# Optimization experiments

Measured on AMD Instinct MI355X. Metric: run time of the kernel, lower is better.

## Reference

```python
import jax, jax.numpy as jnp
import numpy as np
import math

WS = 8      # window size
HEADS = 8

def _layer_norm(x, g, b, eps=1e-5):
    m = jnp.mean(x, -1, keepdims=True)
    v = jnp.var(x, -1, keepdims=True)
    return (x - m) / jnp.sqrt(v + eps) * g + b

def _freqs_cis_2d(dim, end, theta=10000.0):
    # 2D axial RoPE: half the rotary dims encode row, half encode column of a sqrt(end) grid
    H = int(math.sqrt(end))
    nf = dim // 4
    freqs = 1.0 / (theta ** (np.arange(0, dim, 4)[:nf].astype(np.float32) / dim))
    f = np.outer(np.arange(H, dtype=np.float32), freqs)          # [H, dim/4]
    fh = np.broadcast_to(f[:, None, :], (H, H, nf))
    fw = np.broadcast_to(f[None, :, :], (H, H, nf))
    ang = np.concatenate([fh, fw], -1).reshape(end, dim // 2)    # [end, dim/2]
    return jnp.asarray(np.cos(ang)), jnp.asarray(np.sin(ang))

def _apply_rope(t, cos, sin):
    # t: [B, n, h, d], cos/sin: [n, d/2]; adjacent pairs form complex numbers (torch view_as_complex)
    tr, ti = t[..., 0::2], t[..., 1::2]
    c = cos[None, :, None, :]
    s = sin[None, :, None, :]
    outr = tr * c - ti * s
    outi = tr * s + ti * c
    return jnp.stack([outr, outi], -1).reshape(t.shape)

def _rel_pos_index(ws):
    coords = np.stack(np.meshgrid(np.arange(ws), np.arange(ws), indexing='ij')).reshape(2, -1)
    rel = (coords[:, :, None] - coords[:, None, :]).transpose(1, 2, 0)
    rel[..., 0] += ws - 1
    rel[..., 1] += ws - 1
    rel[..., 0] *= 2 * ws - 1
    return rel.sum(-1)  # [ws^2, ws^2]

def _rel_coords_table(ws):
    r = np.arange(-(ws - 1), ws, dtype=np.float32)
    t = np.stack(np.meshgrid(r, r, indexing='ij'), -1)  # [2ws-1, 2ws-1, 2]
    t = t / (ws - 1)
    t = t * 8.0
    t = np.sign(t) * np.log2(np.abs(t) + 1.0) / np.log2(8.0)
    return t.reshape(-1, 2)

def _cosine_attn(q, k, v, ls, bias=None):
    # v2 attention: cosine-normalized QK with clamped learnable logit scale
    qn = q / jnp.clip(jnp.linalg.norm(q, axis=-1, keepdims=True), 1e-12)
    kn = k / jnp.clip(jnp.linalg.norm(k, axis=-1, keepdims=True), 1e-12)
    a = jnp.einsum('bhnd,bhmd->bhnm', qn, kn) * jnp.exp(jnp.minimum(ls, 4.6052))
    if bias is not None:
        a = a + bias
    a = jax.nn.softmax(a, -1)
    return jnp.einsum('bhnm,bhmd->bhnd', a, v)

def _window_partition(x, ws):
    B, H, W, C = x.shape
    x = x.reshape(B, H // ws, ws, W // ws, ws, C).transpose(0, 1, 3, 2, 4, 5)
    return x.reshape(-1, ws * ws, C)

def _window_reverse(xw, ws, H, W, C):
    x = xw.reshape(-1, H // ws, W // ws, ws, ws, C).transpose(0, 1, 3, 2, 4, 5)
    return x.reshape(-1, H, W, C)

def setup_inputs() -> dict:
    key = jax.random.key(0)
    ks = jax.random.split(key, 12)
    B, H, W, C, heads, mr = 8, 64, 64, 512, HEADS, 4
    nct = (H // WS) * (W // WS)  # one carrier token per window, 8x8 grid
    s = 0.02
    d = {}
    d['x'] = jax.random.normal(ks[0], (B, H, W, C), jnp.float32)
    d['ct'] = jax.random.normal(ks[1], (B, nct, C), jnp.float32)
    d['w_qkv_ct'] = jax.random.normal(ks[2], (C, 3 * C), jnp.float32) * s
    d['logit_scale_ct'] = jnp.full((heads, 1, 1), float(np.log(10.0)), jnp.float32)
    d['ln_g_ct1'] = jnp.ones(C); d['ln_b_ct1'] = jnp.zeros(C)
    d['ln_g_ct2'] = jnp.ones(C); d['ln_b_ct2'] = jnp.zeros(C)
    d['mlp_ct_w1'] = jax.random.normal(ks[3], (C, mr * C), jnp.float32) * s
    d['mlp_ct_b1'] = jnp.zeros(mr * C)
    d['mlp_ct_w2'] = jax.random.normal(ks[4], (mr * C, C), jnp.float32) * s
    d['mlp_ct_b2'] = jnp.zeros(C)
    d['w_qkv_win'] = jax.random.normal(ks[5], (C, 3 * C), jnp.float32) * s
    d['w_proj_win'] = jax.random.normal(ks[6], (C, C), jnp.float32) * s
    d['b_proj_win'] = jnp.zeros(C)
    d['logit_scale_win'] = jnp.full((heads, 1, 1), float(np.log(10.0)), jnp.float32)
    d['ln_g_w1'] = jnp.ones(C); d['ln_b_w1'] = jnp.zeros(C)
    d['ln_g_w2'] = jnp.ones(C); d['ln_b_w2'] = jnp.zeros(C)
    d['cpb_w1'] = jax.random.normal(ks[7], (2, 512), jnp.float32) * s
    d['cpb_b1'] = jnp.zeros(512)
    d['cpb_w2'] = jax.random.normal(ks[8], (512, heads), jnp.float32) * s
    d['mlp_w_w1'] = jax.random.normal(ks[9], (C, mr * C), jnp.float32) * s
    d['mlp_w_b1'] = jnp.zeros(mr * C)
    d['mlp_w_w2'] = jax.random.normal(ks[10], (mr * C, C), jnp.float32) * s
    d['mlp_w_b2'] = jnp.zeros(C)
    return d

def reference(x, ct, w_qkv_ct, logit_scale_ct, ln_g_ct1, ln_b_ct1, ln_g_ct2, ln_b_ct2,
              mlp_ct_w1, mlp_ct_b1, mlp_ct_w2, mlp_ct_b2,
              w_qkv_win, w_proj_win, b_proj_win, logit_scale_win,
              ln_g_w1, ln_b_w1, ln_g_w2, ln_b_w2,
              cpb_w1, cpb_b1, cpb_w2,
              mlp_w_w1, mlp_w_b1, mlp_w_w2, mlp_w_b2):
    B, H, W, C = x.shape
    heads = HEADS
    hd = C // heads
    n_ct = ct.shape[1]

    # ---- carrier-token global attention (RoPE2d + cosine-scaled QK, v2) ----
    h = _layer_norm(ct, ln_g_ct1, ln_b_ct1)
    q, k, v = jnp.split(h @ w_qkv_ct, 3, -1)
    q = q.reshape(B, n_ct, heads, hd)
    k = k.reshape(B, n_ct, heads, hd)
    cos, sin = _freqs_cis_2d(hd, n_ct)
    q = _apply_rope(q, cos, sin).transpose(0, 2, 1, 3)   # [B,h,n,d]
    k = _apply_rope(k, cos, sin).transpose(0, 2, 1, 3)
    v = v.reshape(B, n_ct, heads, hd).transpose(0, 2, 1, 3)
    o = _cosine_attn(q, k, v, logit_scale_ct)
    ct = ct + o.transpose(0, 2, 1, 3).reshape(B, n_ct, C)
    h = _layer_norm(ct, ln_g_ct2, ln_b_ct2)
    ct = ct + (jax.nn.gelu(h @ mlp_ct_w1 + mlp_ct_b1, approximate=False) @ mlp_ct_w2 + mlp_ct_b2)

    # ---- windowed local attention with carrier token prepended per window ----
    xw = _window_partition(x, WS)          # [B*nW, ws^2, C]
    ctw = ct.reshape(-1, 1, C)             # carrier token for each window
    z = jnp.concatenate([ctw, xw], 1)      # [B*nW, 1+ws^2, C]
    N = z.shape[1]
    h2 = _layer_norm(z, ln_g_w1, ln_b_w1)
    q, k, v = jnp.split(h2 @ w_qkv_win, 3, -1)
    q = q.reshape(-1, N, heads, hd).transpose(0, 2, 1, 3)
    k = k.reshape(-1, N, heads, hd).transpose(0, 2, 1, 3)
    v = v.reshape(-1, N, heads, hd).transpose(0, 2, 1, 3)

    # Swin-v2 log-CPB relative position bias, zero-padded for the global (carrier) token
    table = jnp.asarray(_rel_coords_table(WS))
    tb = jax.nn.relu(table @ cpb_w1 + cpb_b1) @ cpb_w2          # [(2ws-1)^2, heads]
    rpi = _rel_pos_index(WS).reshape(-1)
    bias = tb[rpi].reshape(WS * WS, WS * WS, heads).transpose(2, 0, 1)
    bias = 16.0 * jax.nn.sigmoid(bias)
    ng = N - WS * WS
    bias = jnp.pad(bias, ((0, 0), (ng, 0), (ng, 0)))

    o = _cosine_attn(q, k, v, logit_scale_win, bias[None])
    o = o.transpose(0, 2, 1, 3).reshape(-1, N, C)
    z = z + (o @ w_proj_win + b_proj_win)
    h2 = _layer_norm(z, ln_g_w2, ln_b_w2)
    z = z + (jax.nn.gelu(h2 @ mlp_w_w1 + mlp_w_b1, approximate=False) @ mlp_w_w2 + mlp_w_b2)

    x_out = _window_reverse(z[:, 1:, :], WS, H, W, C)   # [B,H,W,C]
    return x_out
```

## Files before the change

### kernel.cpp

```cpp
#include <hip/hip_runtime.h>
#include <math.h>

typedef __bf16 bf16x8 __attribute__((ext_vector_type(8)));
typedef float f32x4 __attribute__((ext_vector_type(4)));

__device__ __forceinline__ unsigned short f2b(float f) {
    unsigned u = __float_as_uint(f);
    u += 0x7fffu + ((u >> 16) & 1u);
    return (unsigned short)(u >> 16);
}
__device__ __forceinline__ float b2f(unsigned short h) {
    return __uint_as_float(((unsigned)h) << 16);
}
__device__ __forceinline__ float gelu_exact(float x) {
    return 0.5f * x * (1.0f + erff(x * 0.70710678118654752f));
}
__device__ __forceinline__ void gl_lds16(const unsigned short* g, unsigned short* l) {
    __builtin_amdgcn_global_load_lds(
        (__attribute__((address_space(1))) const void*)g,
        (__attribute__((address_space(3))) void*)l, 16, 0, 0);
}

__global__ void transpose_f2b(const float* __restrict__ in,
                              unsigned short* __restrict__ out, int R, int Cc) {
    __shared__ float tile[32][33];
    int c0 = blockIdx.x * 32, r0 = blockIdx.y * 32;
    int tx = threadIdx.x & 31, ty = threadIdx.x >> 5;
    for (int i = ty; i < 32; i += 8)
        tile[i][tx] = in[(size_t)(r0 + i) * Cc + c0 + tx];
    __syncthreads();
    for (int i = ty; i < 32; i += 8)
        out[(size_t)(c0 + i) * R + r0 + tx] = f2b(tile[tx][i]);
}

template<int INBF>
__global__ __launch_bounds__(256) void ln_bf16(const void* __restrict__ xin,
    const float* __restrict__ g, const float* __restrict__ bb,
    unsigned short* __restrict__ out)
{
    int tok = blockIdx.x, t = threadIdx.x;
    float v0, v1;
    if (INBF) {
        unsigned u = ((const unsigned*)xin)[(size_t)tok * 256 + t];
        v0 = b2f((unsigned short)(u & 0xffff));
        v1 = b2f((unsigned short)(u >> 16));
    } else {
        float2 f = ((const float2*)xin)[(size_t)tok * 256 + t];
        v0 = f.x; v1 = f.y;
    }
    float s = v0 + v1, sq = v0 * v0 + v1 * v1;
    for (int off = 32; off; off >>= 1) {
        s  += __shfl_down(s, off);
        sq += __shfl_down(sq, off);
    }
    __shared__ float red[8];
    if ((t & 63) == 0) { red[t >> 6] = s; red[4 + (t >> 6)] = sq; }
    __syncthreads();
    float S  = red[0] + red[1] + red[2] + red[3];
    float SQ = red[4] + red[5] + red[6] + red[7];
    float mean = S * (1.0f / 512.0f);
    float var  = SQ * (1.0f / 512.0f) - mean * mean;
    float rstd = rsqrtf(var + 1e-5f);
    int c = t * 2;
    float y0 = (v0 - mean) * rstd * g[c]     + bb[c];
    float y1 = (v1 - mean) * rstd * g[c + 1] + bb[c + 1];
    ((unsigned*)out)[(size_t)tok * 256 + t] = (unsigned)f2b(y0) | ((unsigned)f2b(y1) << 16);
}

template<int ACT, int BIAS, int RESID, int OUTBF>
__global__ __launch_bounds__(256) void gemm_bf16k(
    const unsigned short* __restrict__ A, const unsigned short* __restrict__ Bt,
    const float* __restrict__ bias, const void* Rres,
    void* Cout, int M, int N, int K)
{
    __shared__ __align__(16) unsigned short As[128 * 32];
    __shared__ __align__(16) unsigned short Bs[128 * 32];
    int t = threadIdx.x;
    int bm = blockIdx.y, bn = blockIdx.x;
    int wave = t >> 6, lane = t & 63;
    int wm = wave >> 1, wn = wave & 1;
    int l15 = lane & 15, kg = lane >> 4;
    f32x4 acc[4][4];
    #pragma unroll
    for (int i = 0; i < 4; i++)
        #pragma unroll
        for (int j = 0; j < 4; j++)
            acc[i][j] = (f32x4){0.f, 0.f, 0.f, 0.f};
    int r0 = t >> 2, c0 = (t & 3) * 8;
    const unsigned short* ga = A  + (size_t)(bm * 128) * K + (size_t)r0 * K + c0;
    const unsigned short* gb = Bt + (size_t)(bn * 128) * K + (size_t)r0 * K + c0;
    unsigned short* la = As + t * 8;
    unsigned short* lb = Bs + t * 8;
    for (int kt = 0; kt < K; kt += 32) {
        gl_lds16(ga + kt, la);
        gl_lds16(ga + kt + (size_t)64 * K, la + 2048);
        gl_lds16(gb + kt, lb);
        gl_lds16(gb + kt + (size_t)64 * K, lb + 2048);
        __syncthreads();
        bf16x8 aF[4], bF[4];
        #pragma unroll
        for (int i = 0; i < 4; i++)
            aF[i] = *(const bf16x8*)&As[(wm * 64 + i * 16 + l15) * 32 + kg * 8];
        #pragma unroll
        for (int j = 0; j < 4; j++)
            bF[j] = *(const bf16x8*)&Bs[(wn * 64 + j * 16 + l15) * 32 + kg * 8];
        #pragma unroll
        for (int i = 0; i < 4; i++)
            #pragma unroll
            for (int j = 0; j < 4; j++)
                acc[i][j] = __builtin_amdgcn_mfma_f32_16x16x32_bf16(aF[i], bF[j], acc[i][j], 0, 0, 0);
        __syncthreads();
    }
    #pragma unroll
    for (int i = 0; i < 4; i++) {
        #pragma unroll
        for (int j = 0; j < 4; j++) {
            #pragma unroll
            for (int rg = 0; rg < 4; rg++) {
                int row = bm * 128 + wm * 64 + i * 16 + kg * 4 + rg;
                int col = bn * 128 + wn * 64 + j * 16 + l15;
                float v = acc[i][j][rg];
                if (BIAS) v += bias[col];
                if (ACT == 1) v = gelu_exact(v);
                if (RESID == 1) v += ((const float*)Rres)[(size_t)row * N + col];
                if (RESID == 2) v += b2f(((const unsigned short*)Rres)[(size_t)row * N + col]);
                if (OUTBF) ((unsigned short*)Cout)[(size_t)row * N + col] = f2b(v);
                else       ((float*)Cout)[(size_t)row * N + col] = v;
            }
        }
    }
}

__global__ __launch_bounds__(256) void rope_qkv_ct(
    const float* __restrict__ qkv, const float* __restrict__ ls,
    float* __restrict__ qn, float* __restrict__ kn, float* __restrict__ vout)
{
    int tok = blockIdx.x;
    int b = tok >> 6, p = tok & 63;
    int t = threadIdx.x;
    int h = t >> 5, r = t & 31;
    const float* base = qkv + (size_t)tok * 1536;
    float q0 = base[h * 64 + 2 * r], q1 = base[h * 64 + 2 * r + 1];
    float k0 = base[512 + h * 64 + 2 * r], k1 = base[512 + h * 64 + 2 * r + 1];
    int i = p >> 3, j = p & 7;
    int f = (r < 16) ? r : (r - 16);
    float mult = (r < 16) ? (float)i : (float)j;
    float freq = expf(-(float)f * (logf(10000.0f) / 16.0f));
    float ang = mult * freq;
    float sn, cs; sincosf(ang, &sn, &cs);
    float qr0 = q0 * cs - q1 * sn, qr1 = q0 * sn + q1 * cs;
    float kr0 = k0 * cs - k1 * sn, kr1 = k0 * sn + k1 * cs;
    float sq = qr0 * qr0 + qr1 * qr1;
    float sk = kr0 * kr0 + kr1 * kr1;
    for (int off = 16; off; off >>= 1) {
        sq += __shfl_xor(sq, off, 32);
        sk += __shfl_xor(sk, off, 32);
    }
    float scale = expf(fminf(ls[h], 4.6052f));
    float qf = scale / fmaxf(sqrtf(sq), 1e-12f);
    float kf = 1.0f  / fmaxf(sqrtf(sk), 1e-12f);
    size_t o = (((size_t)(b * 8 + h) * 64) + p) * 64 + 2 * r;
    qn[o] = qr0 * qf; qn[o + 1] = qr1 * qf;
    kn[o] = kr0 * kf; kn[o + 1] = kr1 * kf;
    int c0 = 2 * t;
    int vh = c0 >> 6, vd = c0 & 63;
    size_t vo = (((size_t)(b * 8 + vh) * 64) + p) * 64 + vd;
    vout[vo]     = base[1024 + c0];
    vout[vo + 1] = base[1024 + c0 + 1];
}

__global__ __launch_bounds__(256) void attn_ct(
    const float* __restrict__ qn, const float* __restrict__ kn, const float* __restrict__ v,
    const float* __restrict__ ct_in, float* __restrict__ ct_out)
{
    int bh = blockIdx.x; int b = bh >> 3, h = bh & 7;
    int t = threadIdx.x;
    __shared__ __align__(16) float Sq[64 * 64];
    __shared__ __align__(16) float Sk[64 * 64];
    __shared__ __align__(16) float Ss[64 * 64];
    const float* qb = qn + (size_t)bh * 4096;
    const float* kb = kn + (size_t)bh * 4096;
    const float* vb = v  + (size_t)bh * 4096;
    for (int idx = t; idx < 1024; idx += 256) {
        ((float4*)Sq)[idx] = ((const float4*)qb)[idx];
        ((float4*)Sk)[idx] = ((const float4*)kb)[idx];
    }
    __syncthreads();
    int i = t >> 2, q4 = t & 3;
    {
        float acc[16];
        #pragma unroll
        for (int jj = 0; jj < 16; jj++) acc[jj] = 0.f;
        for (int k = 0; k < 64; k++) {
            float qv = Sq[i * 64 + k];
            #pragma unroll
            for (int jj = 0; jj < 16; jj++)
                acc[jj] += qv * Sk[(q4 * 16 + jj) * 64 + k];
        }
        float mx = -1e30f;
        #pragma unroll
        for (int jj = 0; jj < 16; jj++) mx = fmaxf(mx, acc[jj]);
        for (int off = 1; off < 4; off <<= 1) mx = fmaxf(mx, __shfl_xor(mx, off, 4));
        float sum = 0.f;
        #pragma unroll
        for (int jj = 0; jj < 16; jj++) { acc[jj] = expf(acc[jj] - mx); sum += acc[jj]; }
        for (int off = 1; off < 4; off <<= 1) sum += __shfl_xor(sum, off, 4);
        float inv = 1.f / sum;
        #pragma unroll
        for (int jj = 0; jj < 16; jj++) Ss[i * 64 + q4 * 16 + jj] = acc[jj] * inv;
    }
    __syncthreads();
    {
        int d0 = q4 * 16;
        float acc[16];
        #pragma unroll
        for (int dd = 0; dd < 16; dd++) acc[dd] = 0.f;
        for (int j = 0; j < 64; j++) {
            float pP = Ss[i * 64 + j];
            #pragma unroll
            for (int dd = 0; dd < 16; dd++) acc[dd] += pP * vb[j * 64 + d0 + dd];
        }
        size_t orow = ((size_t)(b * 64 + i)) * 512 + h * 64 + d0;
        #pragma unroll
        for (int dd = 0; dd < 16; dd++) ct_out[orow + dd] = ct_in[orow + dd] + acc[dd];
    }
}

__global__ void assemble_z(const float* __restrict__ x, const float* __restrict__ ctf,
                           unsigned short* __restrict__ z) {
    int gid = blockIdx.x * 256 + threadIdx.x;
    if (gid >= 512 * 65 * 128) return;
    int c4 = gid & 127, tk = gid >> 7;
    int win = tk / 65, tok = tk - win * 65;
    float4 v;
    if (tok == 0) {
        v = ((const float4*)ctf)[(size_t)win * 128 + c4];
    } else {
        int p = tok - 1;
        int b = win >> 6, wh = (win >> 3) & 7, ww = win & 7;
        size_t pix = ((size_t)(b * 64 + wh * 8 + (p >> 3)) * 64) + ww * 8 + (p & 7);
        v = ((const float4*)x)[pix * 128 + c4];
    }
    ushort4 u;
    u.x = f2b(v.x); u.y = f2b(v.y); u.z = f2b(v.z); u.w = f2b(v.w);
    ((ushort4*)z)[gid] = u;
}

__global__ void cpb_tb(const float* __restrict__ w1, const float* __restrict__ b1,
                       const float* __restrict__ w2, float* __restrict__ tb) {
    int pos = blockIdx.x;
    int t = threadIdx.x;
    int a = pos / 15, bq = pos % 15;
    float t0 = ((float)(a  - 7)) / 7.0f * 8.0f;
    float t1 = ((float)(bq - 7)) / 7.0f * 8.0f;
    float l8 = log2f(8.0f);
    float x0 = copysignf(log2f(fabsf(t0) + 1.0f) / l8, t0);
    float x1 = copysignf(log2f(fabsf(t1) + 1.0f) / l8, t1);
    __shared__ float acc8[8];
    if (t < 8) acc8[t] = 0.f;
    __syncthreads();
    float partial[8] = {0, 0, 0, 0, 0, 0, 0, 0};
    for (int u = t; u < 512; u += 256) {
        float hv = fmaxf(x0 * w1[u] + x1 * w1[512 + u] + b1[u], 0.0f);
        #pragma unroll
        for (int hh = 0; hh < 8; hh++) partial[hh] += hv * w2[u * 8 + hh];
    }
    for (int hh = 0; hh < 8; hh++) atomicAdd(&acc8[hh], partial[hh]);
    __syncthreads();
    if (t < 8) tb[pos * 8 + t] = acc8[t];
}

__global__ void bias_fill(const float* __restrict__ tb, float* __restrict__ bias) {
    int idx = blockIdx.x * 256 + threadIdx.x;
    if (idx >= 8 * 65 * 65) return;
    int h = idx / 4225, rem = idx % 4225;
    int i = rem / 65, j = rem % 65;
    float val = 0.f;
    if (i > 0 && j > 0) {
        int ii = i - 1, jj = j - 1;
        int d0 = (ii >> 3) - (jj >> 3) + 7;
        int d1 = (ii & 7) - (jj & 7) + 7;
        float xv = tb[(d0 * 15 + d1) * 8 + h];
        val = 16.0f / (1.0f + expf(-xv));
    }
    bias[idx] = val;
}

__global__ __launch_bounds__(256) void attn_win(
    const unsigned short* __restrict__ qkv, const float* __restrict__ ls,
    const float* __restrict__ bias, unsigned short* __restrict__ obuf)
{
    int win = blockIdx.x >> 3, h = blockIdx.x & 7;
    int t = threadIdx.x;
    int wave = t >> 6, lane = t & 63, l15 = lane & 15, kg = lane >> 4;
    __shared__ __align__(16) unsigned short U[11520];
    __shared__ __align__(16) unsigned short SvT[64 * 104];
    __shared__ __align__(16) float Ss[65 * 68];
    __shared__ float qfac[65], kfac[65];
    unsigned short* Sq = U;
    unsigned short* Sk = U + 5760;
    unsigned short* Sp = U;

    for (int idx = t; idx < 15 * 18; idx += 256) {
        int r = 65 + idx / 18, c4 = (idx % 18) * 4;
        *(ushort4*)&Sq[r * 72 + c4] = (ushort4){0, 0, 0, 0};
        *(ushort4*)&Sk[r * 72 + c4] = (ushort4){0, 0, 0, 0};
    }
    for (int idx = t; idx < 64 * 26; idx += 256)
        *(ushort4*)&SvT[idx * 4] = (ushort4){0, 0, 0, 0};
    __syncthreads();
    const unsigned short* base = qkv + (size_t)win * 65 * 1536 + h * 64;
    for (int idx = t; idx < 65 * 16; idx += 256) {
        int r = idx >> 4, d4 = (idx & 15) * 4;
        const unsigned short* rp = base + (size_t)r * 1536 + d4;
        ushort4 uq = *(const ushort4*)rp;
        ushort4 uk = *(const ushort4*)(rp + 512);
        ushort4 uv = *(const ushort4*)(rp + 1024);
        *(ushort4*)&Sq[r * 72 + d4] = uq;
        *(ushort4*)&Sk[r * 72 + d4] = uk;
        SvT[(d4 + 0) * 104 + r] = uv.x;
        SvT[(d4 + 1) * 104 + r] = uv.y;
        SvT[(d4 + 2) * 104 + r] = uv.z;
        SvT[(d4 + 3) * 104 + r] = uv.w;
    }
    __syncthreads();
    if (t < 130) {
        int r = (t < 65) ? t : (t - 65);
        const unsigned short* row = ((t < 65) ? Sq : Sk) + r * 72;
        float s = 0.f;
        for (int d = 0; d < 64; d++) { float v = b2f(row[d]); s += v * v; }
        float f = 1.0f / fmaxf(sqrtf(s), 1e-12f);
        if (t < 65) qfac[r] = f * expf(fminf(ls[h], 4.6052f));
        else        kfac[r] = f;
    }
    __syncthreads();
    for (int s = wave; s < 25; s += 4) {
        int tm = s / 5, tn = s % 5;
        f32x4 acc = (f32x4){0.f, 0.f, 0.f, 0.f};
        #pragma unroll
        for (int kk = 0; kk < 2; kk++) {
            bf16x8 aF = *(const bf16x8*)&Sq[(tm * 16 + l15) * 72 + kk * 32 + kg * 8];
            bf16x8 bF = *(const bf16x8*)&Sk[(tn * 16 + l15) * 72 + kk * 32 + kg * 8];
            acc = __builtin_amdgcn_mfma_f32_16x16x32_bf16(aF, bF, acc, 0, 0, 0);
        }
        #pragma unroll
        for (int rg = 0; rg < 4; rg++) {
            int i = tm * 16 + kg * 4 + rg, j = tn * 16 + l15;
            if (i < 65 && j < 65)
                Ss[i * 68 + j] = acc[rg] * qfac[i] * kfac[j] + bias[(size_t)h * 4225 + i * 65 + j];
        }
    }
    __syncthreads();
    for (int idx = t; idx < 80 * 26; idx += 256)
        *(ushort4*)&Sp[idx * 4] = (ushort4){0, 0, 0, 0};
    __syncthreads();
    if (t < 65) {
        float mx = -1e30f;
        for (int j = 0; j < 65; j++) mx = fmaxf(mx, Ss[t * 68 + j]);
        float sum = 0.f;
        for (int j = 0; j < 65; j++) { float e = expf(Ss[t * 68 + j] - mx); Ss[t * 68 + j] = e; sum += e; }
        float inv = 1.f / sum;
        for (int j = 0; j < 65; j++) Sp[t * 104 + j] = f2b(Ss[t * 68 + j] * inv);
    }
    __syncthreads();
    for (int s = wave; s < 20; s += 4) {
        int tm = s >> 2, tn = s & 3;
        f32x4 acc = (f32x4){0.f, 0.f, 0.f, 0.f};
        #pragma unroll
        for (int kk = 0; kk < 3; kk++) {
            bf16x8 aF = *(const bf16x8*)&Sp[(tm * 16 + l15) * 104 + kk * 32 + kg * 8];
            bf16x8 bF = *(const bf16x8*)&SvT[(tn * 16 + l15) * 104 + kk * 32 + kg * 8];
            acc = __builtin_amdgcn_mfma_f32_16x16x32_bf16(aF, bF, acc, 0, 0, 0);
        }
        #pragma unroll
        for (int rg = 0; rg < 4; rg++) {
            int i = tm * 16 + kg * 4 + rg, d = tn * 16 + l15;
            if (i < 65)
                obuf[((size_t)(win * 65 + i)) * 512 + h * 64 + d] = f2b(acc[rg]);
        }
    }
}

__global__ void reverse_z(const unsigned short* __restrict__ z, float* __restrict__ out) {
    int gid = blockIdx.x * 256 + threadIdx.x;
    if (gid >= 8 * 64 * 64 * 128) return;
    int c4 = gid & 127, pix = gid >> 7;
    int b = pix >> 12, rem = pix & 4095;
    int hh = rem >> 6, w_ = rem & 63;
    int win = b * 64 + (hh >> 3) * 8 + (w_ >> 3);
    int tok = 1 + (hh & 7) * 8 + (w_ & 7);
    ushort4 u = ((const ushort4*)z)[((size_t)(win * 65 + tok)) * 128 + c4];
    float4 v;
    v.x = b2f(u.x); v.y = b2f(u.y); v.z = b2f(u.z); v.w = b2f(u.w);
    ((float4*)out)[gid] = v;
}

extern "C" void kernel_launch(void* const* d_in, const int* in_sizes, int n_in,
                              void* d_out, int out_size, void* d_ws, size_t ws_size,
                              hipStream_t stream)
{
    const float* x        = (const float*)d_in[0];
    const float* ct       = (const float*)d_in[1];
    const float* w_qkv_ct = (const float*)d_in[2];
    const float* ls_ct    = (const float*)d_in[3];
    const float* g_ct1    = (const float*)d_in[4];
    const float* b_ct1    = (const float*)d_in[5];
    const float* g_ct2    = (const float*)d_in[6];
    const float* b_ct2    = (const float*)d_in[7];
    const float* w1_ct    = (const float*)d_in[8];
    const float* b1_ct    = (const float*)d_in[9];
    const float* w2_ct    = (const float*)d_in[10];
    const float* b2_ct    = (const float*)d_in[11];
    const float* w_qkv_w  = (const float*)d_in[12];
    const float* w_proj   = (const float*)d_in[13];
    const float* b_proj   = (const float*)d_in[14];
    const float* ls_w     = (const float*)d_in[15];
    const float* g_w1     = (const float*)d_in[16];
    const float* b_w1     = (const float*)d_in[17];
    const float* g_w2     = (const float*)d_in[18];
    const float* b_w2     = (const float*)d_in[19];
    const float* cpb_w1   = (const float*)d_in[20];
    const float* cpb_b1   = (const float*)d_in[21];
    const float* cpb_w2   = (const float*)d_in[22];
    const float* w1_w     = (const float*)d_in[23];
    const float* b1_w     = (const float*)d_in[24];
    const float* w2_w     = (const float*)d_in[25];
    const float* b2_w     = (const float*)d_in[26];

    char* wsb = (char*)d_ws;
    size_t off = 0;
    auto alloc = [&](size_t bytes) -> void* {
        void* p = (void*)(wsb + off);
        off += (bytes + 255) & ~((size_t)255);
        return p;
    };
    unsigned short* wqkvct_t = (unsigned short*)alloc((size_t)1536 * 512 * 2);
    unsigned short* w1ct_t   = (unsigned short*)alloc((size_t)2048 * 512 * 2);
    unsigned short* w2ct_t   = (unsigned short*)alloc((size_t)512 * 2048 * 2);
    unsigned short* wqkvw_t  = (unsigned short*)alloc((size_t)1536 * 512 * 2);
    unsigned short* wproj_t  = (unsigned short*)alloc((size_t)512 * 512 * 2);
    unsigned short* w1w_t    = (unsigned short*)alloc((size_t)2048 * 512 * 2);
    unsigned short* w2w_t    = (unsigned short*)alloc((size_t)512 * 2048 * 2);
    unsigned short* h_ct     = (unsigned short*)alloc((size_t)512 * 512 * 2);
    float* qkv_ct  = (float*)alloc((size_t)512 * 1536 * 4);
    float* qn_ct   = (float*)alloc((size_t)8 * 8 * 64 * 64 * 4);
    float* kn_ct   = (float*)alloc((size_t)8 * 8 * 64 * 64 * 4);
    float* v_ct    = (float*)alloc((size_t)8 * 8 * 64 * 64 * 4);
    float* ct_work = (float*)alloc((size_t)512 * 512 * 4);
    unsigned short* midc = (unsigned short*)alloc((size_t)512 * 2048 * 2);
    float* tb    = (float*)alloc((size_t)225 * 8 * 4);
    float* biasw = (float*)alloc((size_t)8 * 65 * 65 * 4);
    unsigned short* z    = (unsigned short*)alloc((size_t)33280 * 512 * 2);
    unsigned short* h2c  = (unsigned short*)alloc((size_t)8320 * 512 * 2);
    unsigned short* qkvc = (unsigned short*)alloc((size_t)8320 * 1536 * 2);
    unsigned short* obufc = (unsigned short*)alloc((size_t)8320 * 512 * 2);
    unsigned short* midw = qkvc;

    transpose_f2b<<<dim3(48, 16), 256, 0, stream>>>(w_qkv_ct, wqkvct_t, 512, 1536);
    transpose_f2b<<<dim3(64, 16), 256, 0, stream>>>(w1_ct, w1ct_t, 512, 2048);
    transpose_f2b<<<dim3(16, 64), 256, 0, stream>>>(w2_ct, w2ct_t, 2048, 512);
    transpose_f2b<<<dim3(48, 16), 256, 0, stream>>>(w_qkv_w, wqkvw_t, 512, 1536);
    transpose_f2b<<<dim3(16, 16), 256, 0, stream>>>(w_proj, wproj_t, 512, 512);
    transpose_f2b<<<dim3(64, 16), 256, 0, stream>>>(w1_w, w1w_t, 512, 2048);
    transpose_f2b<<<dim3(16, 64), 256, 0, stream>>>(w2_w, w2w_t, 2048, 512);

    ln_bf16<0><<<512, 256, 0, stream>>>(ct, g_ct1, b_ct1, h_ct);
    gemm_bf16k<0, 0, 0, 0><<<dim3(12, 4), 256, 0, stream>>>(h_ct, wqkvct_t, nullptr, nullptr, qkv_ct, 512, 1536, 512);
    rope_qkv_ct<<<512, 256, 0, stream>>>(qkv_ct, ls_ct, qn_ct, kn_ct, v_ct);
    attn_ct<<<64, 256, 0, stream>>>(qn_ct, kn_ct, v_ct, ct, ct_work);
    ln_bf16<0><<<512, 256, 0, stream>>>(ct_work, g_ct2, b_ct2, h_ct);
    gemm_bf16k<1, 1, 0, 1><<<dim3(16, 4), 256, 0, stream>>>(h_ct, w1ct_t, b1_ct, nullptr, midc, 512, 2048, 512);
    gemm_bf16k<0, 1, 1, 0><<<dim3(4, 4), 256, 0, stream>>>(midc, w2ct_t, b2_ct, ct_work, ct_work, 512, 512, 2048);

    assemble_z<<<16640, 256, 0, stream>>>(x, ct_work, z);
    cpb_tb<<<225, 256, 0, stream>>>(cpb_w1, cpb_b1, cpb_w2, tb);
    bias_fill<<<133, 256, 0, stream>>>(tb, biasw);

    for (int c = 0; c < 4; c++) {
        size_t rowoff = (size_t)c * 8320;
        ln_bf16<1><<<8320, 256, 0, stream>>>(z + rowoff * 512, g_w1, b_w1, h2c);
        gemm_bf16k<0, 0, 0, 1><<<dim3(12, 65), 256, 0, stream>>>(h2c, wqkvw_t, nullptr, nullptr, qkvc, 8320, 1536, 512);
        attn_win<<<1024, 256, 0, stream>>>(qkvc, ls_w, biasw, obufc);
        gemm_bf16k<0, 1, 2, 1><<<dim3(4, 65), 256, 0, stream>>>(obufc, wproj_t, b_proj, z + rowoff * 512, z + rowoff * 512, 8320, 512, 512);
    }
    for (int c = 0; c < 4; c++) {
        size_t rowoff = (size_t)c * 8320;
        ln_bf16<1><<<8320, 256, 0, stream>>>(z + rowoff * 512, g_w2, b_w2, h2c);
        gemm_bf16k<1, 1, 0, 1><<<dim3(16, 65), 256, 0, stream>>>(h2c, w1w_t, b1_w, nullptr, midw, 8320, 2048, 512);
        gemm_bf16k<0, 1, 2, 1><<<dim3(4, 65), 256, 0, stream>>>(midw, w2w_t, b2_w, z + rowoff * 512, z + rowoff * 512, 8320, 512, 2048);
    }
    reverse_z<<<16384, 256, 0, stream>>>(z, (float*)d_out);
}
```

Measured before the change: 1.201 ms.

## Double-buffer GEMM LDS tiles with K=64 steps and enlarge window-stage chunks

```diff
diff --git a/kernel.cpp b/kernel.cpp
--- a/kernel.cpp
+++ b/kernel.cpp
@@ -73,8 +73,8 @@
     const float* __restrict__ bias, const void* Rres,
     void* Cout, int M, int N, int K)
 {
-    __shared__ __align__(16) unsigned short As[128 * 32];
-    __shared__ __align__(16) unsigned short Bs[128 * 32];
+    __shared__ __align__(16) unsigned short As[2][2][128 * 32];
+    __shared__ __align__(16) unsigned short Bs[2][2][128 * 32];
     int t = threadIdx.x;
     int bm = blockIdx.y, bn = blockIdx.x;
     int wave = t >> 6, lane = t & 63;
@@ -87,29 +87,38 @@
         for (int j = 0; j < 4; j++)
             acc[i][j] = (f32x4){0.f, 0.f, 0.f, 0.f};
     int r0 = t >> 2, c0 = (t & 3) * 8;
-    const unsigned short* ga = A  + (size_t)(bm * 128) * K + (size_t)r0 * K + c0;
-    const unsigned short* gb = Bt + (size_t)(bn * 128) * K + (size_t)r0 * K + c0;
-    unsigned short* la = As + t * 8;
-    unsigned short* lb = Bs + t * 8;
-    for (int kt = 0; kt < K; kt += 32) {
-        gl_lds16(ga + kt, la);
-        gl_lds16(ga + kt + (size_t)64 * K, la + 2048);
-        gl_lds16(gb + kt, lb);
-        gl_lds16(gb + kt + (size_t)64 * K, lb + 2048);
+    const unsigned short* gA = A  + (size_t)(bm * 128 + r0) * K + c0;
+    const unsigned short* gB = Bt + (size_t)(bn * 128 + r0) * K + c0;
+    auto stage = [&](int p, int kt) {
+        #pragma unroll
+        for (int kh = 0; kh < 2; kh++) {
+            gl_lds16(gA + kt + kh * 32,                  &As[p][kh][t * 8]);
+            gl_lds16(gA + kt + kh * 32 + (size_t)64 * K, &As[p][kh][t * 8 + 2048]);
+            gl_lds16(gB + kt + kh * 32,                  &Bs[p][kh][t * 8]);
+            gl_lds16(gB + kt + kh * 32 + (size_t)64 * K, &Bs[p][kh][t * 8 + 2048]);
+        }
+    };
+    stage(0, 0);
+    int p = 0;
+    for (int kt = 0; kt < K; kt += 64) {
         __syncthreads();
-        bf16x8 aF[4], bF[4];
-        #pragma unroll
-        for (int i = 0; i < 4; i++)
-            aF[i] = *(const bf16x8*)&As[(wm * 64 + i * 16 + l15) * 32 + kg * 8];
-        #pragma unroll
-        for (int j = 0; j < 4; j++)
-            bF[j] = *(const bf16x8*)&Bs[(wn * 64 + j * 16 + l15) * 32 + kg * 8];
-        #pragma unroll
-        for (int i = 0; i < 4; i++)
+        if (kt + 64 < K) stage(p ^ 1, kt + 64);
+        #pragma unroll
+        for (int kh = 0; kh < 2; kh++) {
+            bf16x8 aF[4], bF[4];
+            #pragma unroll
+            for (int i = 0; i < 4; i++)
+                aF[i] = *(const bf16x8*)&As[p][kh][(wm * 64 + i * 16 + l15) * 32 + kg * 8];
             #pragma unroll
             for (int j = 0; j < 4; j++)
-                acc[i][j] = __builtin_amdgcn_mfma_f32_16x16x32_bf16(aF[i], bF[j], acc[i][j], 0, 0, 0);
-        __syncthreads();
+                bF[j] = *(const bf16x8*)&Bs[p][kh][(wn * 64 + j * 16 + l15) * 32 + kg * 8];
+            #pragma unroll
+            for (int i = 0; i < 4; i++)
+                #pragma unroll
+                for (int j = 0; j < 4; j++)
+                    acc[i][j] = __builtin_amdgcn_mfma_f32_16x16x32_bf16(aF[i], bF[j], acc[i][j], 0, 0, 0);
+        }
+        p ^= 1;
     }
     #pragma unroll
     for (int i = 0; i < 4; i++) {
@@ -429,65 +438,80 @@
 
     char* wsb = (char*)d_ws;
     size_t off = 0;
-    auto alloc = [&](size_t bytes) -> void* {
-        void* p = (void*)(wsb + off);
+    auto alloc = [&](size_t bytes) -> char* {
+        char* p = wsb + off;
         off += (bytes + 255) & ~((size_t)255);
         return p;
     };
-    unsigned short* wqkvct_t = (unsigned short*)alloc((size_t)1536 * 512 * 2);
-    unsigned short* w1ct_t   = (unsigned short*)alloc((size_t)2048 * 512 * 2);
-    unsigned short* w2ct_t   = (unsigned short*)alloc((size_t)512 * 2048 * 2);
-    unsigned short* wqkvw_t  = (unsigned short*)alloc((size_t)1536 * 512 * 2);
-    unsigned short* wproj_t  = (unsigned short*)alloc((size_t)512 * 512 * 2);
-    unsigned short* w1w_t    = (unsigned short*)alloc((size_t)2048 * 512 * 2);
-    unsigned short* w2w_t    = (unsigned short*)alloc((size_t)512 * 2048 * 2);
-    unsigned short* h_ct     = (unsigned short*)alloc((size_t)512 * 512 * 2);
-    float* qkv_ct  = (float*)alloc((size_t)512 * 1536 * 4);
-    float* qn_ct   = (float*)alloc((size_t)8 * 8 * 64 * 64 * 4);
-    float* kn_ct   = (float*)alloc((size_t)8 * 8 * 64 * 64 * 4);
-    float* v_ct    = (float*)alloc((size_t)8 * 8 * 64 * 64 * 4);
+    unsigned short* wqkvw_t = (unsigned short*)alloc((size_t)1536 * 512 * 2);
+    unsigned short* wproj_t = (unsigned short*)alloc((size_t)512 * 512 * 2);
+    unsigned short* w1w_t   = (unsigned short*)alloc((size_t)2048 * 512 * 2);
+    unsigned short* w2w_t   = (unsigned short*)alloc((size_t)512 * 2048 * 2);
     float* ct_work = (float*)alloc((size_t)512 * 512 * 4);
-    unsigned short* midc = (unsigned short*)alloc((size_t)512 * 2048 * 2);
-    float* tb    = (float*)alloc((size_t)225 * 8 * 4);
-    float* biasw = (float*)alloc((size_t)8 * 65 * 65 * 4);
-    unsigned short* z    = (unsigned short*)alloc((size_t)33280 * 512 * 2);
-    unsigned short* h2c  = (unsigned short*)alloc((size_t)8320 * 512 * 2);
-    unsigned short* qkvc = (unsigned short*)alloc((size_t)8320 * 1536 * 2);
-    unsigned short* obufc = (unsigned short*)alloc((size_t)8320 * 512 * 2);
-    unsigned short* midw = qkvc;
-
-    transpose_f2b<<<dim3(48, 16), 256, 0, stream>>>(w_qkv_ct, wqkvct_t, 512, 1536);
-    transpose_f2b<<<dim3(64, 16), 256, 0, stream>>>(w1_ct, w1ct_t, 512, 2048);
-    transpose_f2b<<<dim3(16, 64), 256, 0, stream>>>(w2_ct, w2ct_t, 2048, 512);
-    transpose_f2b<<<dim3(48, 16), 256, 0, stream>>>(w_qkv_w, wqkvw_t, 512, 1536);
-    transpose_f2b<<<dim3(16, 16), 256, 0, stream>>>(w_proj, wproj_t, 512, 512);
-    transpose_f2b<<<dim3(64, 16), 256, 0, stream>>>(w1_w, w1w_t, 512, 2048);
-    transpose_f2b<<<dim3(16, 64), 256, 0, stream>>>(w2_w, w2w_t, 2048, 512);
-
-    ln_bf16<0><<<512, 256, 0, stream>>>(ct, g_ct1, b_ct1, h_ct);
-    gemm_bf16k<0, 0, 0, 0><<<dim3(12, 4), 256, 0, stream>>>(h_ct, wqkvct_t, nullptr, nullptr, qkv_ct, 512, 1536, 512);
-    rope_qkv_ct<<<512, 256, 0, stream>>>(qkv_ct, ls_ct, qn_ct, kn_ct, v_ct);
-    attn_ct<<<64, 256, 0, stream>>>(qn_ct, kn_ct, v_ct, ct, ct_work);
-    ln_bf16<0><<<512, 256, 0, stream>>>(ct_work, g_ct2, b_ct2, h_ct);
-    gemm_bf16k<1, 1, 0, 1><<<dim3(16, 4), 256, 0, stream>>>(h_ct, w1ct_t, b1_ct, nullptr, midc, 512, 2048, 512);
-    gemm_bf16k<0, 1, 1, 0><<<dim3(4, 4), 256, 0, stream>>>(midc, w2ct_t, b2_ct, ct_work, ct_work, 512, 512, 2048);
+    float* tb      = (float*)alloc((size_t)225 * 8 * 4);
+    float* biasw   = (float*)alloc((size_t)8 * 65 * 65 * 4);
+    unsigned short* z = (unsigned short*)alloc((size_t)33280 * 512 * 2);
+    size_t ubase = off;
+
+    size_t need2 = ubase + (size_t)16640 * 5120 + 4096;
+    int CH = (ws_size >= need2) ? 16640 : 8320;
+    int nc = 33280 / CH, NB = CH / 128;
+
+    unsigned short* h2c   = (unsigned short*)(wsb + ubase);
+    unsigned short* qkvc  = (unsigned short*)(wsb + ubase + (size_t)CH * 1024);
+    unsigned short* obufc = h2c;
+    unsigned short* midw  = qkvc;
+
+    {
+        size_t coff = ubase;
+        auto calloc_ = [&](size_t bytes) -> char* {
+            char* p = wsb + coff;
+            coff += (bytes + 255) & ~((size_t)255);
+            return p;
+        };
+        unsigned short* wqkvct_t = (unsigned short*)calloc_((size_t)1536 * 512 * 2);
+        unsigned short* w1ct_t   = (unsigned short*)calloc_((size_t)2048 * 512 * 2);
+        unsigned short* w2ct_t   = (unsigned short*)calloc_((size_t)512 * 2048 * 2);
+        unsigned short* h_ct     = (unsigned short*)calloc_((size_t)512 * 512 * 2);
+        float* qkv_ct = (float*)calloc_((size_t)512 * 1536 * 4);
+        float* qn_ct  = (float*)calloc_((size_t)8 * 8 * 64 * 64 * 4);
+        float* kn_ct  = (float*)calloc_((size_t)8 * 8 * 64 * 64 * 4);
+        float* v_ct   = (float*)calloc_((size_t)8 * 8 * 64 * 64 * 4);
+        unsigned short* midc = (unsigned short*)calloc_((size_t)512 * 2048 * 2);
+
+        transpose_f2b<<<dim3(48, 16), 256, 0, stream>>>(w_qkv_ct, wqkvct_t, 512, 1536);
+        transpose_f2b<<<dim3(64, 16), 256, 0, stream>>>(w1_ct, w1ct_t, 512, 2048);
+        transpose_f2b<<<dim3(16, 64), 256, 0, stream>>>(w2_ct, w2ct_t, 2048, 512);
+        transpose_f2b<<<dim3(48, 16), 256, 0, stream>>>(w_qkv_w, wqkvw_t, 512, 1536);
+        transpose_f2b<<<dim3(16, 16), 256, 0, stream>>>(w_proj, wproj_t, 512, 512);
+        transpose_f2b<<<dim3(64, 16), 256, 0, stream>>>(w1_w, w1w_t, 512, 2048);
+        transpose_f2b<<<dim3(16, 64), 256, 0, stream>>>(w2_w, w2w_t, 2048, 512);
+
+        ln_bf16<0><<<512, 256, 0, stream>>>(ct, g_ct1, b_ct1, h_ct);
+        gemm_bf16k<0, 0, 0, 0><<<dim3(12, 4), 256, 0, stream>>>(h_ct, wqkvct_t, nullptr, nullptr, qkv_ct, 512, 1536, 512);
+        rope_qkv_ct<<<512, 256, 0, stream>>>(qkv_ct, ls_ct, qn_ct, kn_ct, v_ct);
+        attn_ct<<<64, 256, 0, stream>>>(qn_ct, kn_ct, v_ct, ct, ct_work);
+        ln_bf16<0><<<512, 256, 0, stream>>>(ct_work, g_ct2, b_ct2, h_ct);
+        gemm_bf16k<1, 1, 0, 1><<<dim3(16, 4), 256, 0, stream>>>(h_ct, w1ct_t, b1_ct, nullptr, midc, 512, 2048, 512);
+        gemm_bf16k<0, 1, 1, 0><<<dim3(4, 4), 256, 0, stream>>>(midc, w2ct_t, b2_ct, ct_work, ct_work, 512, 512, 2048);
+    }
 
     assemble_z<<<16640, 256, 0, stream>>>(x, ct_work, z);
     cpb_tb<<<225, 256, 0, stream>>>(cpb_w1, cpb_b1, cpb_w2, tb);
     bias_fill<<<133, 256, 0, stream>>>(tb, biasw);
 
-    for (int c = 0; c < 4; c++) {
-        size_t rowoff = (size_t)c * 8320;
-        ln_bf16<1><<<8320, 256, 0, stream>>>(z + rowoff * 512, g_w1, b_w1, h2c);
-        gemm_bf16k<0, 0, 0, 1><<<dim3(12, 65), 256, 0, stream>>>(h2c, wqkvw_t, nullptr, nullptr, qkvc, 8320, 1536, 512);
-        attn_win<<<1024, 256, 0, stream>>>(qkvc, ls_w, biasw, obufc);
-        gemm_bf16k<0, 1, 2, 1><<<dim3(4, 65), 256, 0, stream>>>(obufc, wproj_t, b_proj, z + rowoff * 512, z + rowoff * 512, 8320, 512, 512);
-    }
-    for (int c = 0; c < 4; c++) {
-        size_t rowoff = (size_t)c * 8320;
-        ln_bf16<1><<<8320, 256, 0, stream>>>(z + rowoff * 512, g_w2, b_w2, h2c);
-        gemm_bf16k<1, 1, 0, 1><<<dim3(16, 65), 256, 0, stream>>>(h2c, w1w_t, b1_w, nullptr, midw, 8320, 2048, 512);
-        gemm_bf16k<0, 1, 2, 1><<<dim3(4, 65), 256, 0, stream>>>(midw, w2w_t, b2_w, z + rowoff * 512, z + rowoff * 512, 8320, 512, 2048);
+    for (int c = 0; c < nc; c++) {
+        size_t rowoff = (size_t)c * CH;
+        ln_bf16<1><<<CH, 256, 0, stream>>>(z + rowoff * 512, g_w1, b_w1, h2c);
+        gemm_bf16k<0, 0, 0, 1><<<dim3(12, NB), 256, 0, stream>>>(h2c, wqkvw_t, nullptr, nullptr, qkvc, CH, 1536, 512);
+        attn_win<<<(CH / 65) * 8, 256, 0, stream>>>(qkvc, ls_w, biasw, obufc);
+        gemm_bf16k<0, 1, 2, 1><<<dim3(4, NB), 256, 0, stream>>>(obufc, wproj_t, b_proj, z + rowoff * 512, z + rowoff * 512, CH, 512, 512);
+    }
+    for (int c = 0; c < nc; c++) {
+        size_t rowoff = (size_t)c * CH;
+        ln_bf16<1><<<CH, 256, 0, stream>>>(z + rowoff * 512, g_w2, b_w2, h2c);
+        gemm_bf16k<1, 1, 0, 1><<<dim3(16, NB), 256, 0, stream>>>(h2c, w1w_t, b1_w, nullptr, midw, CH, 2048, 512);
+        gemm_bf16k<0, 1, 2, 1><<<dim3(4, NB), 256, 0, stream>>>(midw, w2w_t, b2_w, z + rowoff * 512, z + rowoff * 512, CH, 512, 2048);
     }
     reverse_z<<<16384, 256, 0, stream>>>(z, (float*)d_out);
 }
```

Measured after the change: 1.047 ms. 1.15x faster.
